# Kernel optimization log

Hardware: AMD Instinct MI355X
Metric: run time of the kernel (lower is better)

The kernel has to match this reference:

```python
import jax, jax.numpy as jnp
import numpy as np

N_NODES = 50000
N_EDGES = 800000
D = 128
DEPTH = 3


def setup_inputs() -> dict:
    key = jax.random.key(0)
    ks = jax.random.split(key, 10)
    s = 1.0 / np.sqrt(D)
    return {
        "h": jax.random.normal(ks[0], (N_NODES, D), dtype=jnp.float32),
        "src": jax.random.randint(ks[1], (N_EDGES,), 0, N_NODES, dtype=jnp.int32),
        "dst": jax.random.randint(ks[2], (N_EDGES,), 0, N_NODES, dtype=jnp.int32),
        "W_in1": jax.random.normal(ks[3], (D, D), dtype=jnp.float32) * s,
        "b_in1": jnp.zeros((D,), dtype=jnp.float32),
        "W_in2": jax.random.normal(ks[4], (D, D), dtype=jnp.float32) * s,
        "b_in2": jnp.zeros((D,), dtype=jnp.float32),
        "W_self": jax.random.normal(ks[5], (DEPTH, D, D), dtype=jnp.float32) * s,
        "b_self": jnp.zeros((DEPTH, D), dtype=jnp.float32),
        "W_neigh": jax.random.normal(ks[6], (DEPTH, D, D), dtype=jnp.float32) * s,
    }


def _mean_aggregate(h, src, dst, n_nodes):
    # gather source features along edges, sum into destination, divide by in-degree
    msg = h[src]                                             # [E, D]
    summed = jax.ops.segment_sum(msg, dst, num_segments=n_nodes)  # [N, D]
    deg = jax.ops.segment_sum(jnp.ones_like(dst, dtype=h.dtype), dst,
                              num_segments=n_nodes)          # [N]
    return summed / jnp.maximum(deg, 1.0)[:, None]


def reference(h, src, dst, W_in1, b_in1, W_in2, b_in2, W_self, b_self, W_neigh):
    n_nodes = h.shape[0]
    # fc_in: Linear -> tanh -> Linear
    h = jnp.tanh(h @ W_in1 + b_in1) @ W_in2 + b_in2
    # stacked SAGEConv(mean) layers with SiLU between layers
    for i in range(DEPTH):
        h_neigh = _mean_aggregate(h, src, dst, n_nodes)
        h = h @ W_self[i] + b_self[i] + h_neigh @ W_neigh[i]
        if i < DEPTH - 1:
            h = jax.nn.silu(h)
    return jnp.tanh(h)
```

## Files before the change

kernel.cpp:

```cpp
#include <hip/hip_runtime.h>
#include <stdint.h>

#define DD 128
#define LDSROW 136

typedef __attribute__((ext_vector_type(8))) short short8;
typedef __attribute__((ext_vector_type(4))) float float4v;

__device__ __forceinline__ unsigned short f2bf(float f) {
  unsigned u = __float_as_uint(f);
  unsigned r = u + 0x7fffu + ((u >> 16) & 1u);
  return (unsigned short)(r >> 16);
}
__device__ __forceinline__ unsigned pack2(float a, float b) {
  return (unsigned)f2bf(a) | ((unsigned)f2bf(b) << 16);
}
__device__ __forceinline__ float2 unpack2(unsigned p) {
  float2 r;
  r.x = __uint_as_float(p << 16);
  r.y = __uint_as_float(p & 0xffff0000u);
  return r;
}

__global__ __launch_bounds__(256) void k_deg_prep(const int* __restrict__ dst, int* deg, int e, int eb,
                                                  const float* __restrict__ W1, const float* __restrict__ W2,
                                                  const float* __restrict__ Wself, const float* __restrict__ Wneigh,
                                                  unsigned* __restrict__ wfrag) {
  int b = blockIdx.x;
  if (b < eb) {
    int i = b * 256 + threadIdx.x;
    if (i < e) atomicAdd(&deg[dst[i]], 1);
  } else {
    int gid = (b - eb) * 256 + threadIdx.x;
    int m = gid >> 13;
    int r = gid & 8191;
    int p = r & 3;
    int lane = (r >> 2) & 63;
    int t = (r >> 8) & 3;
    int c = r >> 10;
    const float* W;
    if (m == 0) W = W1;
    else if (m == 1) W = W2;
    else if (m < 5) W = Wself + (size_t)(m - 2) * DD * DD;
    else W = Wneigh + (size_t)(m - 5) * DD * DD;
    int n = c * 16 + (lane & 15);
    int k = t * 32 + (lane >> 4) * 8 + 2 * p;
    wfrag[gid] = pack2(W[(size_t)k * DD + n], W[(size_t)(k + 1) * DD + n]);
  }
}

__global__ __launch_bounds__(1024) void k_scan1(const int* __restrict__ deg, int* __restrict__ incl,
                                                int* __restrict__ bsum, int n) {
  __shared__ int sh[1024];
  int t = threadIdx.x;
  int i = blockIdx.x * 1024 + t;
  int v = (i < n) ? deg[i] : 0;
  sh[t] = v;
  __syncthreads();
#pragma unroll
  for (int off = 1; off < 1024; off <<= 1) {
    int add = (t >= off) ? sh[t - off] : 0;
    __syncthreads();
    sh[t] += add;
    __syncthreads();
  }
  if (i < n) incl[i] = sh[t];
  if (t == 1023) bsum[blockIdx.x] = sh[1023];
}

__global__ __launch_bounds__(1024) void k_scan3(const int* __restrict__ deg, const int* __restrict__ incl,
                                                const int* __restrict__ bsum, int* __restrict__ rowstart,
                                                int* __restrict__ cursor, int n, int nb) {
  __shared__ int sboff;
  int t = threadIdx.x;
  if (t < 64) {
    int orig = (t < nb) ? bsum[t] : 0;
    int v = orig;
#pragma unroll
    for (int off = 1; off < 64; off <<= 1) {
      int u = __shfl_up(v, off);
      if (t >= off) v += u;
    }
    if (t == (int)blockIdx.x) sboff = v - orig;
  }
  __syncthreads();
  int i = blockIdx.x * 1024 + t;
  if (i >= n) return;
  int d = deg[i];
  int excl = sboff + incl[i] - d;
  rowstart[i] = excl;
  cursor[i] = excl;
  if (i == n - 1) rowstart[n] = excl + d;
}

__global__ __launch_bounds__(256) void k_fill_r(const int* __restrict__ src, const int* __restrict__ dst,
                                                int* cursor, int* __restrict__ esrc, int e, int rstep) {
  int range = blockIdx.x & 7;
  int i = (blockIdx.x >> 3) * 256 + threadIdx.x;
  if (i >= e) return;
  int d = dst[i];
  int lo = range * rstep;
  if (d >= lo && d < lo + rstep) {
    int p = atomicAdd(&cursor[d], 1);
    esrc[p] = src[i];
  }
}

__global__ __launch_bounds__(256) void k_aggr(const uint4* __restrict__ h, const int* __restrict__ rowstart,
                                              const int* __restrict__ esrc, uint4* __restrict__ out, int n) {
  int wave = threadIdx.x >> 6, lane = threadIdx.x & 63;
  int g = lane >> 4, nn = lane & 15;
  int r = blockIdx.x * 4 + wave;
  if (r >= n) return;
  int ru = __builtin_amdgcn_readfirstlane(r);
  int beg = rowstart[ru], end = rowstart[ru + 1];
  int cnt = end - beg;
  float acc[8];
#pragma unroll
  for (int i = 0; i < 8; ++i) acc[i] = 0.f;
  int base = 0;
  for (; base + 16 <= cnt; base += 16) {
    int j0 = beg + base + g;
    int s0 = esrc[j0];
    int s1 = esrc[j0 + 4];
    int s2 = esrc[j0 + 8];
    int s3 = esrc[j0 + 12];
    uint4 v0 = h[(size_t)s0 * 16 + nn];
    uint4 v1 = h[(size_t)s1 * 16 + nn];
    uint4 v2 = h[(size_t)s2 * 16 + nn];
    uint4 v3 = h[(size_t)s3 * 16 + nn];
    const unsigned* u0 = (const unsigned*)&v0;
    const unsigned* u1 = (const unsigned*)&v1;
    const unsigned* u2 = (const unsigned*)&v2;
    const unsigned* u3 = (const unsigned*)&v3;
#pragma unroll
    for (int k = 0; k < 4; ++k) {
      float2 f0 = unpack2(u0[k]), f1 = unpack2(u1[k]);
      float2 f2 = unpack2(u2[k]), f3 = unpack2(u3[k]);
      acc[2 * k]     += (f0.x + f1.x) + (f2.x + f3.x);
      acc[2 * k + 1] += (f0.y + f1.y) + (f2.y + f3.y);
    }
  }
  for (; base + 8 <= cnt; base += 8) {
    int j0 = beg + base + g;
    int s0 = esrc[j0];
    int s1 = esrc[j0 + 4];
    uint4 v0 = h[(size_t)s0 * 16 + nn];
    uint4 v1 = h[(size_t)s1 * 16 + nn];
    const unsigned* u0 = (const unsigned*)&v0;
    const unsigned* u1 = (const unsigned*)&v1;
#pragma unroll
    for (int k = 0; k < 4; ++k) {
      float2 f0 = unpack2(u0[k]), f1 = unpack2(u1[k]);
      acc[2 * k] += f0.x + f1.x;
      acc[2 * k + 1] += f0.y + f1.y;
    }
  }
  if (base + g < cnt) {
    int s = esrc[beg + base + g];
    uint4 v = h[(size_t)s * 16 + nn];
    const unsigned* u = (const unsigned*)&v;
#pragma unroll
    for (int k = 0; k < 4; ++k) {
      float2 f = unpack2(u[k]);
      acc[2 * k] += f.x;
      acc[2 * k + 1] += f.y;
    }
  }
  if (base + 4 + g < cnt) {
    int s = esrc[beg + base + 4 + g];
    uint4 v = h[(size_t)s * 16 + nn];
    const unsigned* u = (const unsigned*)&v;
#pragma unroll
    for (int k = 0; k < 4; ++k) {
      float2 f = unpack2(u[k]);
      acc[2 * k] += f.x;
      acc[2 * k + 1] += f.y;
    }
  }
#pragma unroll
  for (int k = 0; k < 8; ++k) {
    acc[k] += __shfl_xor(acc[k], 16, 64);
    acc[k] += __shfl_xor(acc[k], 32, 64);
  }
  if (g == 0) {
    float inv = 1.0f / (float)(cnt > 1 ? cnt : 1);
    uint4 o;
    o.x = pack2(acc[0] * inv, acc[1] * inv);
    o.y = pack2(acc[2] * inv, acc[3] * inv);
    o.z = pack2(acc[4] * inv, acc[5] * inv);
    o.w = pack2(acc[6] * inv, acc[7] * inv);
    out[(size_t)r * 16 + nn] = o;
  }
}

__global__ __launch_bounds__(256) void k_fc12(const float* __restrict__ h,
                                              const uint4* __restrict__ wf1, const uint4* __restrict__ wf2,
                                              const float* __restrict__ b1, const float* __restrict__ b2,
                                              unsigned short* __restrict__ outbf, int n) {
  __shared__ unsigned short sT[64 * LDSROW];
  int tid = threadIdx.x, w = tid >> 6, lane = tid & 63;
  int q = lane >> 4, nn = lane & 15;
  int r0 = (blockIdx.x * 4 + w) * 16;
  int rr = r0 + nn; if (rr >= n) rr = n - 1;
  short8 a[4];
  {
    const float* X = h + (size_t)rr * DD;
#pragma unroll
    for (int t = 0; t < 4; ++t) {
      int k0 = t * 32 + q * 8;
      float4 f0 = *(const float4*)&X[k0];
      float4 f1 = *(const float4*)&X[k0 + 4];
      uint4 u;
      u.x = pack2(f0.x, f0.y); u.y = pack2(f0.z, f0.w);
      u.z = pack2(f1.x, f1.y); u.w = pack2(f1.z, f1.w);
      a[t] = __builtin_bit_cast(short8, u);
    }
  }
  float4v acc[8];
#pragma unroll
  for (int c = 0; c < 8; ++c) acc[c] = (float4v){0.f, 0.f, 0.f, 0.f};
#pragma unroll
  for (int c = 0; c < 8; ++c) {
#pragma unroll
    for (int t = 0; t < 4; ++t) {
      short8 b = __builtin_bit_cast(short8, wf1[(c * 4 + t) * 64 + lane]);
      acc[c] = __builtin_amdgcn_mfma_f32_16x16x32_bf16(a[t], b, acc[c], 0, 0, 0);
    }
  }
#pragma unroll
  for (int c = 0; c < 8; ++c) {
    float bc = b1[c * 16 + nn];
#pragma unroll
    for (int g = 0; g < 4; ++g) {
      int lr = w * 16 + q * 4 + g;
      sT[lr * LDSROW + c * 16 + nn] = f2bf(tanhf(acc[c][g] + bc));
    }
  }
  __syncthreads();
  short8 a2[4];
#pragma unroll
  for (int t = 0; t < 4; ++t) {
    const uint4* p = (const uint4*)&sT[(w * 16 + nn) * LDSROW + (t * 4 + q) * 8];
    a2[t] = __builtin_bit_cast(short8, *p);
  }
  float4v acc2[8];
#pragma unroll
  for (int c = 0; c < 8; ++c) acc2[c] = (float4v){0.f, 0.f, 0.f, 0.f};
#pragma unroll
  for (int c = 0; c < 8; ++c) {
#pragma unroll
    for (int t = 0; t < 4; ++t) {
      short8 b = __builtin_bit_cast(short8, wf2[(c * 4 + t) * 64 + lane]);
      acc2[c] = __builtin_amdgcn_mfma_f32_16x16x32_bf16(a2[t], b, acc2[c], 0, 0, 0);
    }
  }
#pragma unroll
  for (int c = 0; c < 8; ++c) {
    float bc = b2[c * 16 + nn];
#pragma unroll
    for (int g = 0; g < 4; ++g) {
      int row = r0 + q * 4 + g;
      if (row < n) outbf[(size_t)row * DD + c * 16 + nn] = f2bf(acc2[c][g] + bc);
    }
  }
}

template <int ACT, bool OUTF32>
__global__ __launch_bounds__(256) void k_sage(const uint4* __restrict__ X, const uint4* __restrict__ G,
                                              const uint4* __restrict__ wfs, const uint4* __restrict__ wfn,
                                              const float* __restrict__ bias, void* __restrict__ outp, int n) {
  int tid = threadIdx.x, w = tid >> 6, lane = tid & 63;
  int q = lane >> 4, nn = lane & 15;
  int r0 = (blockIdx.x * 4 + w) * 16;
  int rr = r0 + nn; if (rr >= n) rr = n - 1;
  short8 a[4], g[4];
  {
    const uint4* Xr = X + (size_t)rr * 16;
    const uint4* Gr = G + (size_t)rr * 16;
#pragma unroll
    for (int t = 0; t < 4; ++t) {
      a[t] = __builtin_bit_cast(short8, Xr[t * 4 + q]);
      g[t] = __builtin_bit_cast(short8, Gr[t * 4 + q]);
    }
  }
  float4v acc[8];
#pragma unroll
  for (int c = 0; c < 8; ++c) acc[c] = (float4v){0.f, 0.f, 0.f, 0.f};
#pragma unroll
  for (int c = 0; c < 8; ++c) {
#pragma unroll
    for (int t = 0; t < 4; ++t) {
      short8 b = __builtin_bit_cast(short8, wfs[(c * 4 + t) * 64 + lane]);
      acc[c] = __builtin_amdgcn_mfma_f32_16x16x32_bf16(a[t], b, acc[c], 0, 0, 0);
    }
#pragma unroll
    for (int t = 0; t < 4; ++t) {
      short8 b = __builtin_bit_cast(short8, wfn[(c * 4 + t) * 64 + lane]);
      acc[c] = __builtin_amdgcn_mfma_f32_16x16x32_bf16(g[t], b, acc[c], 0, 0, 0);
    }
  }
#pragma unroll
  for (int c = 0; c < 8; ++c) {
    float bc = bias[c * 16 + nn];
#pragma unroll
    for (int gg = 0; gg < 4; ++gg) {
      int row = r0 + q * 4 + gg;
      if (row < n) {
        float v = acc[c][gg] + bc;
        if (ACT == 1) v = tanhf(v);
        else v = v / (1.f + __expf(-v));
        if (OUTF32) ((float*)outp)[(size_t)row * DD + c * 16 + nn] = v;
        else ((unsigned short*)outp)[(size_t)row * DD + c * 16 + nn] = f2bf(v);
      }
    }
  }
}

extern "C" void kernel_launch(void* const* d_in, const int* in_sizes, int n_in,
                              void* d_out, int out_size, void* d_ws, size_t ws_size,
                              hipStream_t stream) {
  const float* h_in = (const float*)d_in[0];
  const int* src    = (const int*)d_in[1];
  const int* dst    = (const int*)d_in[2];
  const float* W1   = (const float*)d_in[3];
  const float* b1   = (const float*)d_in[4];
  const float* W2   = (const float*)d_in[5];
  const float* b2   = (const float*)d_in[6];
  const float* Wself  = (const float*)d_in[7];
  const float* bself  = (const float*)d_in[8];
  const float* Wneigh = (const float*)d_in[9];
  const int N = in_sizes[0] / DD;
  const int E = in_sizes[1];
  float* out = (float*)d_out;

  char* ws = (char*)d_ws;
  size_t off = 0;
  auto alloc = [&](size_t bytes) -> char* {
    char* p = ws + off;
    off = (off + bytes + 255) & ~(size_t)255;
    return p;
  };
  unsigned* wfrag = (unsigned*)alloc(8 * 32768);
  unsigned* actA  = (unsigned*)alloc((size_t)N * 64 * 4);
  unsigned* actB  = (unsigned*)alloc((size_t)N * 64 * 4);
  unsigned* neigh = (unsigned*)alloc((size_t)N * 64 * 4);
  int* esrc     = (int*)alloc((size_t)E * 4);
  int* degi     = (int*)alloc((size_t)N * 4);
  int* rowstart = (int*)alloc((size_t)(N + 1) * 4);
  int* cursor   = (int*)alloc((size_t)N * 4);
  int* incl     = (int*)alloc((size_t)N * 4);
  int* bsum     = (int*)alloc(65 * 4);

  hipMemsetAsync(degi, 0, (size_t)N * 4, stream);
  const int eb = (E + 255) / 256;
  const int nb = (N + 1023) / 1024;
  const int rstep = (N + 7) / 8;
  k_deg_prep<<<eb + 256, 256, 0, stream>>>(dst, degi, E, eb, W1, W2, Wself, Wneigh, wfrag);
  k_scan1<<<nb, 1024, 0, stream>>>(degi, incl, bsum, N);
  k_scan3<<<nb, 1024, 0, stream>>>(degi, incl, bsum, rowstart, cursor, N, nb);
  k_fill_r<<<eb * 8, 256, 0, stream>>>(src, dst, cursor, esrc, E, rstep);

  const int gb = (N + 63) / 64;
  const int ab = (N + 3) / 4;
  const uint4* wf = (const uint4*)wfrag;

  k_fc12<<<gb, 256, 0, stream>>>(h_in, wf + 0 * 2048, wf + 1 * 2048, b1, b2,
                                 (unsigned short*)actB, N);

  const unsigned* cur = actB;
  unsigned* nxt = actA;
  for (int l = 0; l < 3; ++l) {
    k_aggr<<<ab, 256, 0, stream>>>((const uint4*)cur, rowstart, esrc, (uint4*)neigh, N);
    const uint4* wsF = wf + (size_t)(2 + l) * 2048;
    const uint4* wnF = wf + (size_t)(5 + l) * 2048;
    const float* bs = bself + (size_t)l * DD;
    if (l < 2) {
      k_sage<2, false><<<gb, 256, 0, stream>>>((const uint4*)cur, (const uint4*)neigh, wsF, wnF, bs, nxt, N);
      const unsigned* tmp = cur;
      cur = nxt;
      nxt = (unsigned*)tmp;
    } else {
      k_sage<1, true><<<gb, 256, 0, stream>>>((const uint4*)cur, (const uint4*)neigh, wsF, wnF, bs, out, N);
    }
  }
}
```

Baseline: 333.5 us.

## Fuse graph preprocessing and input MLP into a persistent megakernel with grid barriers

Replaces the degree count, weight packing, two scan kernels, CSR fill and the fc_in kernel with one persistent 256-block kernel. Phases are separated by atomic grid-wide barriers. The fc_in MLP runs on the blocks left idle during the block scan, and a single memset now zeroes both the degree array and the barrier counters. The goal is to cut launch gaps and overlap the MLP with the scan. The cost is that the design relies on all 256 blocks being co-resident. It also gives fewer threads to the atomic fill phase and puts more register pressure on fc_in under the 1024-thread launch bound.

```diff
diff --git a/kernel.cpp b/kernel.cpp
--- a/kernel.cpp
+++ b/kernel.cpp
@@ -3,6 +3,7 @@
 
 #define DD 128
 #define LDSROW 136
+#define MEGA_BLOCKS 256
 
 typedef __attribute__((ext_vector_type(8))) short short8;
 typedef __attribute__((ext_vector_type(4))) float float4v;
@@ -22,87 +23,187 @@
   return r;
 }
 
-__global__ __launch_bounds__(256) void k_deg_prep(const int* __restrict__ dst, int* deg, int e, int eb,
-                                                  const float* __restrict__ W1, const float* __restrict__ W2,
-                                                  const float* __restrict__ Wself, const float* __restrict__ Wneigh,
-                                                  unsigned* __restrict__ wfrag) {
-  int b = blockIdx.x;
-  if (b < eb) {
-    int i = b * 256 + threadIdx.x;
-    if (i < e) atomicAdd(&deg[dst[i]], 1);
+__device__ __forceinline__ void gridbar(int* bar, int idx, int nblocks) {
+  __syncthreads();
+  if (threadIdx.x == 0) {
+    __threadfence();
+    int arrived = __hip_atomic_fetch_add(&bar[idx], 1, __ATOMIC_ACQ_REL, __HIP_MEMORY_SCOPE_AGENT) + 1;
+    while (arrived < nblocks) {
+      __builtin_amdgcn_s_sleep(2);
+      arrived = __hip_atomic_load(&bar[idx], __ATOMIC_ACQUIRE, __HIP_MEMORY_SCOPE_AGENT);
+    }
+    __threadfence();
+  }
+  __syncthreads();
+}
+
+__global__ __launch_bounds__(1024) void k_mega(
+    const int* __restrict__ src, const int* __restrict__ dst, int e,
+    int* deg, int* __restrict__ incl, int* __restrict__ bsum,
+    int* __restrict__ rowstart, int* cursor, int* __restrict__ esrc, int* bar,
+    const float* __restrict__ W1, const float* __restrict__ W2,
+    const float* __restrict__ Wself, const float* __restrict__ Wneigh,
+    unsigned* __restrict__ wfrag,
+    const float* __restrict__ hin, const float* __restrict__ b1, const float* __restrict__ b2,
+    unsigned short* __restrict__ actB,
+    int n, int nb, int rstep) {
+  __shared__ char smem[4 * 64 * LDSROW * 2];
+  const int b = blockIdx.x, t = threadIdx.x;
+
+  for (int i = b * 1024 + t; i < e; i += MEGA_BLOCKS * 1024) atomicAdd(&deg[dst[i]], 1);
+  {
+    int gid = b * 1024 + t;
+    if (gid < 65536) {
+      int m = gid >> 13;
+      int r = gid & 8191;
+      int p = r & 3;
+      int lane = (r >> 2) & 63;
+      int tt = (r >> 8) & 3;
+      int c = r >> 10;
+      const float* W;
+      if (m == 0) W = W1;
+      else if (m == 1) W = W2;
+      else if (m < 5) W = Wself + (size_t)(m - 2) * DD * DD;
+      else W = Wneigh + (size_t)(m - 5) * DD * DD;
+      int nn = c * 16 + (lane & 15);
+      int k = tt * 32 + (lane >> 4) * 8 + 2 * p;
+      wfrag[gid] = pack2(W[(size_t)k * DD + nn], W[(size_t)(k + 1) * DD + nn]);
+    }
+  }
+  gridbar(bar, 0, MEGA_BLOCKS);
+
+  if (b < nb) {
+    int* sh = (int*)smem;
+    int i = b * 1024 + t;
+    int v = (i < n) ? deg[i] : 0;
+    sh[t] = v;
+    __syncthreads();
+#pragma unroll
+    for (int off = 1; off < 1024; off <<= 1) {
+      int add = (t >= off) ? sh[t - off] : 0;
+      __syncthreads();
+      sh[t] += add;
+      __syncthreads();
+    }
+    if (i < n) incl[i] = sh[t];
+    if (t == 1023) bsum[b] = sh[1023];
   } else {
-    int gid = (b - eb) * 256 + threadIdx.x;
-    int m = gid >> 13;
-    int r = gid & 8191;
-    int p = r & 3;
-    int lane = (r >> 2) & 63;
-    int t = (r >> 8) & 3;
-    int c = r >> 10;
-    const float* W;
-    if (m == 0) W = W1;
-    else if (m == 1) W = W2;
-    else if (m < 5) W = Wself + (size_t)(m - 2) * DD * DD;
-    else W = Wneigh + (size_t)(m - 5) * DD * DD;
-    int n = c * 16 + (lane & 15);
-    int k = t * 32 + (lane >> 4) * 8 + 2 * p;
-    wfrag[gid] = pack2(W[(size_t)k * DD + n], W[(size_t)(k + 1) * DD + n]);
-  }
-}
-
-__global__ __launch_bounds__(1024) void k_scan1(const int* __restrict__ deg, int* __restrict__ incl,
-                                                int* __restrict__ bsum, int n) {
-  __shared__ int sh[1024];
-  int t = threadIdx.x;
-  int i = blockIdx.x * 1024 + t;
-  int v = (i < n) ? deg[i] : 0;
-  sh[t] = v;
-  __syncthreads();
-#pragma unroll
-  for (int off = 1; off < 1024; off <<= 1) {
-    int add = (t >= off) ? sh[t - off] : 0;
+    const uint4* wf1 = (const uint4*)wfrag;
+    const uint4* wf2 = wf1 + 2048;
+    int grp = t >> 8;
+    int tile = (b - nb) * 4 + grp;
+    int ntiles = (n + 63) / 64;
+    bool active = (tile < ntiles);
+    unsigned short* sT = (unsigned short*)(smem + grp * (64 * LDSROW * 2) / 4 * 4);
+    sT = (unsigned short*)smem + (size_t)grp * 64 * LDSROW;
+    int tid256 = t & 255;
+    int w = tid256 >> 6, lane = t & 63;
+    int q = lane >> 4, nn = lane & 15;
+    int r0 = tile * 64 + w * 16;
+    float4v acc2[8];
+    if (active) {
+      int rr = r0 + nn; if (rr >= n) rr = n - 1;
+      short8 a[4];
+      {
+        const float* X = hin + (size_t)rr * DD;
+#pragma unroll
+        for (int tt = 0; tt < 4; ++tt) {
+          int k0 = tt * 32 + q * 8;
+          float4 f0 = *(const float4*)&X[k0];
+          float4 f1 = *(const float4*)&X[k0 + 4];
+          uint4 u;
+          u.x = pack2(f0.x, f0.y); u.y = pack2(f0.z, f0.w);
+          u.z = pack2(f1.x, f1.y); u.w = pack2(f1.z, f1.w);
+          a[tt] = __builtin_bit_cast(short8, u);
+        }
+      }
+      float4v acc[8];
+#pragma unroll
+      for (int c = 0; c < 8; ++c) acc[c] = (float4v){0.f, 0.f, 0.f, 0.f};
+#pragma unroll
+      for (int c = 0; c < 8; ++c) {
+#pragma unroll
+        for (int tt = 0; tt < 4; ++tt) {
+          short8 bb = __builtin_bit_cast(short8, wf1[(c * 4 + tt) * 64 + lane]);
+          acc[c] = __builtin_amdgcn_mfma_f32_16x16x32_bf16(a[tt], bb, acc[c], 0, 0, 0);
+        }
+      }
+#pragma unroll
+      for (int c = 0; c < 8; ++c) {
+        float bc = b1[c * 16 + nn];
+#pragma unroll
+        for (int g = 0; g < 4; ++g) {
+          int lr = w * 16 + q * 4 + g;
+          sT[lr * LDSROW + c * 16 + nn] = f2bf(tanhf(acc[c][g] + bc));
+        }
+      }
+    }
     __syncthreads();
-    sh[t] += add;
+    if (active) {
+      short8 a2[4];
+#pragma unroll
+      for (int tt = 0; tt < 4; ++tt) {
+        const uint4* p = (const uint4*)&sT[(w * 16 + nn) * LDSROW + (tt * 4 + q) * 8];
+        a2[tt] = __builtin_bit_cast(short8, *p);
+      }
+#pragma unroll
+      for (int c = 0; c < 8; ++c) acc2[c] = (float4v){0.f, 0.f, 0.f, 0.f};
+#pragma unroll
+      for (int c = 0; c < 8; ++c) {
+#pragma unroll
+        for (int tt = 0; tt < 4; ++tt) {
+          short8 bb = __builtin_bit_cast(short8, wf2[(c * 4 + tt) * 64 + lane]);
+          acc2[c] = __builtin_amdgcn_mfma_f32_16x16x32_bf16(a2[tt], bb, acc2[c], 0, 0, 0);
+        }
+      }
+#pragma unroll
+      for (int c = 0; c < 8; ++c) {
+        float bc = b2[c * 16 + nn];
+#pragma unroll
+        for (int g = 0; g < 4; ++g) {
+          int row = r0 + q * 4 + g;
+          if (row < n) actB[(size_t)row * DD + c * 16 + nn] = f2bf(acc2[c][g] + bc);
+        }
+      }
+    }
+  }
+  gridbar(bar, 1, MEGA_BLOCKS);
+
+  if (b < nb) {
+    __shared__ int sboff;
+    if (t < 64) {
+      int orig = (t < nb) ? bsum[t] : 0;
+      int v = orig;
+#pragma unroll
+      for (int off = 1; off < 64; off <<= 1) {
+        int u = __shfl_up(v, off);
+        if (t >= off) v += u;
+      }
+      if (t == b) sboff = v - orig;
+    }
     __syncthreads();
-  }
-  if (i < n) incl[i] = sh[t];
-  if (t == 1023) bsum[blockIdx.x] = sh[1023];
-}
-
-__global__ __launch_bounds__(1024) void k_scan3(const int* __restrict__ deg, const int* __restrict__ incl,
-                                                const int* __restrict__ bsum, int* __restrict__ rowstart,
-                                                int* __restrict__ cursor, int n, int nb) {
-  __shared__ int sboff;
-  int t = threadIdx.x;
-  if (t < 64) {
-    int orig = (t < nb) ? bsum[t] : 0;
-    int v = orig;
-#pragma unroll
-    for (int off = 1; off < 64; off <<= 1) {
-      int u = __shfl_up(v, off);
-      if (t >= off) v += u;
-    }
-    if (t == (int)blockIdx.x) sboff = v - orig;
-  }
-  __syncthreads();
-  int i = blockIdx.x * 1024 + t;
-  if (i >= n) return;
-  int d = deg[i];
-  int excl = sboff + incl[i] - d;
-  rowstart[i] = excl;
-  cursor[i] = excl;
-  if (i == n - 1) rowstart[n] = excl + d;
-}
-
-__global__ __launch_bounds__(256) void k_fill_r(const int* __restrict__ src, const int* __restrict__ dst,
-                                                int* cursor, int* __restrict__ esrc, int e, int rstep) {
-  int range = blockIdx.x & 7;
-  int i = (blockIdx.x >> 3) * 256 + threadIdx.x;
-  if (i >= e) return;
-  int d = dst[i];
-  int lo = range * rstep;
-  if (d >= lo && d < lo + rstep) {
-    int p = atomicAdd(&cursor[d], 1);
-    esrc[p] = src[i];
+    int i = b * 1024 + t;
+    if (i < n) {
+      int d = deg[i];
+      int excl = sboff + incl[i] - d;
+      rowstart[i] = excl;
+      cursor[i] = excl;
+      if (i == n - 1) rowstart[n] = excl + d;
+    }
+  }
+  gridbar(bar, 2, MEGA_BLOCKS);
+
+  {
+    int range = b & 7;
+    int sub = b >> 3;
+    int lo = range * rstep, hi = lo + rstep;
+    for (int i = sub * 1024 + t; i < e; i += 32 * 1024) {
+      int d = dst[i];
+      if (d >= lo && d < hi) {
+        int p = atomicAdd(&cursor[d], 1);
+        esrc[p] = src[i];
+      }
+    }
   }
 }
 
@@ -194,78 +295,6 @@
   }
 }
 
-__global__ __launch_bounds__(256) void k_fc12(const float* __restrict__ h,
-                                              const uint4* __restrict__ wf1, const uint4* __restrict__ wf2,
-                                              const float* __restrict__ b1, const float* __restrict__ b2,
-                                              unsigned short* __restrict__ outbf, int n) {
-  __shared__ unsigned short sT[64 * LDSROW];
-  int tid = threadIdx.x, w = tid >> 6, lane = tid & 63;
-  int q = lane >> 4, nn = lane & 15;
-  int r0 = (blockIdx.x * 4 + w) * 16;
-  int rr = r0 + nn; if (rr >= n) rr = n - 1;
-  short8 a[4];
-  {
-    const float* X = h + (size_t)rr * DD;
-#pragma unroll
-    for (int t = 0; t < 4; ++t) {
-      int k0 = t * 32 + q * 8;
-      float4 f0 = *(const float4*)&X[k0];
-      float4 f1 = *(const float4*)&X[k0 + 4];
-      uint4 u;
-      u.x = pack2(f0.x, f0.y); u.y = pack2(f0.z, f0.w);
-      u.z = pack2(f1.x, f1.y); u.w = pack2(f1.z, f1.w);
-      a[t] = __builtin_bit_cast(short8, u);
-    }
-  }
-  float4v acc[8];
-#pragma unroll
-  for (int c = 0; c < 8; ++c) acc[c] = (float4v){0.f, 0.f, 0.f, 0.f};
-#pragma unroll
-  for (int c = 0; c < 8; ++c) {
-#pragma unroll
-    for (int t = 0; t < 4; ++t) {
-      short8 b = __builtin_bit_cast(short8, wf1[(c * 4 + t) * 64 + lane]);
-      acc[c] = __builtin_amdgcn_mfma_f32_16x16x32_bf16(a[t], b, acc[c], 0, 0, 0);
-    }
-  }
-#pragma unroll
-  for (int c = 0; c < 8; ++c) {
-    float bc = b1[c * 16 + nn];
-#pragma unroll
-    for (int g = 0; g < 4; ++g) {
-      int lr = w * 16 + q * 4 + g;
-      sT[lr * LDSROW + c * 16 + nn] = f2bf(tanhf(acc[c][g] + bc));
-    }
-  }
-  __syncthreads();
-  short8 a2[4];
-#pragma unroll
-  for (int t = 0; t < 4; ++t) {
-    const uint4* p = (const uint4*)&sT[(w * 16 + nn) * LDSROW + (t * 4 + q) * 8];
-    a2[t] = __builtin_bit_cast(short8, *p);
-  }
-  float4v acc2[8];
-#pragma unroll
-  for (int c = 0; c < 8; ++c) acc2[c] = (float4v){0.f, 0.f, 0.f, 0.f};
-#pragma unroll
-  for (int c = 0; c < 8; ++c) {
-#pragma unroll
-    for (int t = 0; t < 4; ++t) {
-      short8 b = __builtin_bit_cast(short8, wf2[(c * 4 + t) * 64 + lane]);
-      acc2[c] = __builtin_amdgcn_mfma_f32_16x16x32_bf16(a2[t], b, acc2[c], 0, 0, 0);
-    }
-  }
-#pragma unroll
-  for (int c = 0; c < 8; ++c) {
-    float bc = b2[c * 16 + nn];
-#pragma unroll
-    for (int g = 0; g < 4; ++g) {
-      int row = r0 + q * 4 + g;
-      if (row < n) outbf[(size_t)row * DD + c * 16 + nn] = f2bf(acc2[c][g] + bc);
-    }
-  }
-}
-
 template <int ACT, bool OUTF32>
 __global__ __launch_bounds__(256) void k_sage(const uint4* __restrict__ X, const uint4* __restrict__ G,
                                               const uint4* __restrict__ wfs, const uint4* __restrict__ wfn,
@@ -341,32 +370,31 @@
     off = (off + bytes + 255) & ~(size_t)255;
     return p;
   };
+  int* degi     = (int*)alloc((size_t)N * 4);
+  int* bar      = (int*)alloc(256);
   unsigned* wfrag = (unsigned*)alloc(8 * 32768);
   unsigned* actA  = (unsigned*)alloc((size_t)N * 64 * 4);
   unsigned* actB  = (unsigned*)alloc((size_t)N * 64 * 4);
   unsigned* neigh = (unsigned*)alloc((size_t)N * 64 * 4);
   int* esrc     = (int*)alloc((size_t)E * 4);
-  int* degi     = (int*)alloc((size_t)N * 4);
   int* rowstart = (int*)alloc((size_t)(N + 1) * 4);
   int* cursor   = (int*)alloc((size_t)N * 4);
   int* incl     = (int*)alloc((size_t)N * 4);
-  int* bsum     = (int*)alloc(65 * 4);
-
-  hipMemsetAsync(degi, 0, (size_t)N * 4, stream);
-  const int eb = (E + 255) / 256;
+  int* bsum     = (int*)alloc(256 * 4);
+
   const int nb = (N + 1023) / 1024;
   const int rstep = (N + 7) / 8;
-  k_deg_prep<<<eb + 256, 256, 0, stream>>>(dst, degi, E, eb, W1, W2, Wself, Wneigh, wfrag);
-  k_scan1<<<nb, 1024, 0, stream>>>(degi, incl, bsum, N);
-  k_scan3<<<nb, 1024, 0, stream>>>(degi, incl, bsum, rowstart, cursor, N, nb);
-  k_fill_r<<<eb * 8, 256, 0, stream>>>(src, dst, cursor, esrc, E, rstep);
+
+  size_t zlen = (size_t)((char*)wfrag - (char*)degi);
+  hipMemsetAsync(degi, 0, zlen, stream);
+
+  k_mega<<<MEGA_BLOCKS, 1024, 0, stream>>>(src, dst, E, degi, incl, bsum, rowstart, cursor,
+                                           esrc, bar, W1, W2, Wself, Wneigh, wfrag,
+                                           h_in, b1, b2, (unsigned short*)actB, N, nb, rstep);
 
   const int gb = (N + 63) / 64;
   const int ab = (N + 3) / 4;
   const uint4* wf = (const uint4*)wfrag;
-
-  k_fc12<<<gb, 256, 0, stream>>>(h_in, wf + 0 * 2048, wf + 1 * 2048, b1, b2,
-                                 (unsigned short*)actB, N);
 
   const unsigned* cur = actB;
   unsigned* nxt = actA;
```

New measurement: 437.0 us. 31.0% more time.
